# Optimization experiments

Measured on AMD Instinct MI355X. Metric: run time of the kernel, lower is better.

## Reference

```python
import jax, jax.numpy as jnp
import numpy as np

K = 3          # kernel size
STRIDE = 1
PAD = 1
DIL = 1
K2 = K * K


def setup_inputs() -> dict:
    key = jax.random.key(0)
    ks = jax.random.split(key, 5)
    B, Cin, Cout, H, W = 8, 128, 128, 64, 64
    x = jax.random.normal(ks[0], (B, Cin, H, W), jnp.float32)
    # conv_offset_mask: Conv2d(Cin, 3*dg*K*K=27, 3x3). Original inits to zero;
    # use small random weights so offsets are nonzero sub-pixel shifts.
    w_off = jax.random.normal(ks[1], (3 * K2, Cin, K, K), jnp.float32) * 0.05
    b_off = jax.random.normal(ks[2], (3 * K2,), jnp.float32) * 0.1
    weight = jax.random.normal(ks[3], (Cout, Cin, K, K), jnp.float32) / np.sqrt(Cin * K2)
    bias = jax.random.normal(ks[4], (Cout,), jnp.float32) * 0.1
    return dict(x=x, w_off=w_off, b_off=b_off, weight=weight, bias=bias)


def _conv(x, w, b):
    y = jax.lax.conv_general_dilated(
        x, w, (STRIDE, STRIDE), [(PAD, PAD), (PAD, PAD)],
        dimension_numbers=('NCHW', 'OIHW', 'NCHW'))
    return y + b[None, :, None, None]


def _sample_one(xb, pyb, pxb, mb):
    Cin, Hin, Win = xb.shape
    y0 = jnp.floor(pyb)
    x0 = jnp.floor(pxb)
    wy = pyb - y0   # fractional weights
    wx = pxb - x0
    y0i = y0.astype(jnp.int32)
    x0i = x0.astype(jnp.int32)
    xf = xb.reshape(Cin, -1)

    def g(yi, xi):
        valid = ((yi >= 0) & (yi < Hin) & (xi >= 0) & (xi < Win)).astype(xb.dtype)
        idx = jnp.clip(yi, 0, Hin - 1) * Win + jnp.clip(xi, 0, Win - 1)
        return xf[:, idx] * valid[None]   # [Cin,K2,Ho,Wo]

    v = (g(y0i, x0i) * ((1 - wy) * (1 - wx))[None]
         + g(y0i, x0i + 1) * ((1 - wy) * wx)[None]
         + g(y0i + 1, x0i) * (wy * (1 - wx))[None]
         + g(y0i + 1, x0i + 1) * (wy * wx)[None])
    return v * mb[None]   # modulated columns [Cin,K2,Ho,Wo]


def reference(x, w_off, b_off, weight, bias):
    B, Cin, Hin, Win = x.shape
    Cout = weight.shape[0]
    om = _conv(x, w_off, b_off)                 # [B, 3*K2, Ho, Wo]
    dy = om[:, :K2]
    dx = om[:, K2:2 * K2]
    m = jax.nn.sigmoid(om[:, 2 * K2:])          # modulation mask
    Ho, Wo = dy.shape[2], dy.shape[3]
    kh = jnp.repeat(jnp.arange(K), K)           # [K2] kernel row per tap
    kw = jnp.tile(jnp.arange(K), K)             # [K2] kernel col per tap
    grid_y = jnp.arange(Ho) * STRIDE - PAD
    grid_x = jnp.arange(Wo) * STRIDE - PAD
    py = dy + grid_y[None, None, :, None] + (kh * DIL)[None, :, None, None]
    px = dx + grid_x[None, None, None, :] + (kw * DIL)[None, :, None, None]
    cols = jax.vmap(_sample_one)(x, py, px, m)  # [B,Cin,K2,Ho,Wo]
    out = jnp.einsum('bckhw,ock->bohw', cols, weight.reshape(Cout, Cin, K2))
    return out + bias[None, :, None, None]
```

## Files before the change

kernel.cpp:

```cpp
#include <hip/hip_runtime.h>
#include <math.h>

#define BATCH 8
#define CIN   128
#define COUT  128
#define HH    64
#define WW    64
#define OC    27
#define KDIM  1152
#define CST   228

typedef unsigned short u16;
typedef unsigned int   u32;
typedef __attribute__((ext_vector_type(8))) short bf16x8;
typedef __attribute__((ext_vector_type(4))) float f32x4;

__device__ __forceinline__ float b2f(u16 u) {
    return __uint_as_float((u32)u << 16);
}
__device__ __forceinline__ u16 f2b(float f) {
    u32 u = __float_as_uint(f);
    return (u16)((u + 0x7fffu + ((u >> 16) & 1u)) >> 16);
}
__device__ __forceinline__ float blo(u32 u) { return __uint_as_float(u << 16); }
__device__ __forceinline__ float bhi(u32 u) { return __uint_as_float(u & 0xffff0000u); }
__device__ __forceinline__ u32 cvtpk(float lo, float hi) {
    u32 r;
    asm("v_cvt_pk_bf16_f32 %0, %1, %2" : "=v"(r) : "v"(lo), "v"(hi));
    return r;
}
__device__ __forceinline__ bf16x8 pack8(u32 a, u32 b, u32 c, u32 d) {
    union { u32 u[4]; bf16x8 v; } z;
    z.u[0] = a; z.u[1] = b; z.u[2] = c; z.u[3] = d;
    return z.v;
}

__device__ __forceinline__ int xswiz(int o, int K) { return (o & 7) * K + (o >> 3); }

__global__ __launch_bounds__(256) void k_prep(const float* __restrict__ x,
                                              const float* __restrict__ weight,
                                              const float* __restrict__ w_off,
                                              u16* __restrict__ xtb,
                                              u16* __restrict__ wbf,
                                              u16* __restrict__ wop) {
    __shared__ float tile[64][65];
    int gbid = blockIdx.x;
    int t = threadIdx.x;
    if (gbid < 1024) {
        int bid = xswiz(gbid, 128);
        int b   = bid >> 7;
        int c0  = ((bid >> 6) & 1) << 6;
        int hw0 = (bid & 63) << 6;
        int ln  = t & 63;
        int cq  = t >> 6;
#pragma unroll
        for (int r = 0; r < 16; ++r) {
            int c_l = cq * 16 + r;
            tile[c_l][ln] = x[(((size_t)(b * CIN + c0 + c_l)) << 12) + hw0 + ln];
        }
        __syncthreads();
#pragma unroll
        for (int r = 0; r < 16; ++r) {
            int hw_w = cq * 16 + r;
            xtb[((size_t)(b << 12) + hw0 + hw_w) * 128 + c0 + ln] = f2b(tile[ln][hw_w]);
        }
    } else if (gbid < 1600) {
        int tid = (gbid - 1024) * 256 + t;
        int j  = tid & 7;
        int l  = (tid >> 3) & 63;
        int ni = (tid >> 9) & 7;
        int s  = (tid >> 12) & 3;
        int t9 = tid >> 14;
        int co = ni * 16 + (l & 15);
        int ci = s * 32 + ((l >> 4) << 3) + j;
        wbf[tid] = f2b(weight[co * KDIM + ci * 9 + t9]);
    } else {
        int tid = (gbid - 1600) * 256 + t;
        int j   = tid & 7;
        int l   = (tid >> 3) & 63;
        int ni  = (tid >> 9) & 1;
        int sg  = (tid >> 10) & 3;
        int rest = tid >> 12;
        int t9  = rest % 9;
        int split = rest / 9;
        int co = ni * 16 + (l & 15);
        int ci = sg * 32 + ((l >> 4) << 3) + j;
        float val = (co < OC) ? w_off[co * KDIM + ci * 9 + t9] : 0.f;
        u16 hi = f2b(val);
        u16 lo = f2b(val - b2f(hi));
        wop[tid] = split ? lo : hi;
    }
}

__global__ __launch_bounds__(512, 4) void k_fused(const float* __restrict__ x,
                                                  const u16* __restrict__ xtb,
                                                  const u16* __restrict__ wop,
                                                  const u16* __restrict__ wbf,
                                                  const float* __restrict__ b_off,
                                                  const float* __restrict__ bias,
                                                  float* __restrict__ out) {
    __shared__ __align__(16) char smem[73904];
    float* Xf  = (float*)smem;
    float* red = (float*)(smem + 58368);
    float* omf = (float*)(smem + 66560);

    const int t  = threadIdx.x;
    const int lb = xswiz(blockIdx.x, 64);
    const int b  = lb >> 6;
    const int h  = lb & 63;
    const int l    = t & 63;
    const int wv   = t >> 6;
    const int l15  = l & 15;
    const int lg   = l >> 4;

    {
        const int ntile = wv & 3;
        const int kgrp  = wv >> 2;

        if (t < 192) {
            int ci = t & 63, row = t >> 6;
            int idx = ci * CST + row * 68 + (((ci >> 3) & 3) << 3) + 64;
            *(float4*)(Xf + idx) = make_float4(0.f, 0.f, 0.f, 0.f);
        }

        f32x4 acc0 = {0.f, 0.f, 0.f, 0.f};
        f32x4 acc1 = {0.f, 0.f, 0.f, 0.f};
        float4 st_[6];

        auto stageA_load = [&](int half) {
#pragma unroll
            for (int it = 0; it < 6; ++it) {
                int slot = t + it * 512;
                int pair = slot >> 4, ln16 = slot & 15;
                int row = pair >> 6, ci = pair & 63;
                int grow = h - 1 + row;
                float4 v = make_float4(0.f, 0.f, 0.f, 0.f);
                if ((unsigned)grow < 64u)
                    v = *(const float4*)(x + (((size_t)(b * CIN + half * 64 + ci)) << 12)
                                           + (grow << 6) + ln16 * 4);
                st_[it] = v;
            }
        };
        auto stageA_store = [&]() {
#pragma unroll
            for (int it = 0; it < 6; ++it) {
                int slot = t + it * 512;
                int pair = slot >> 4, ln16 = slot & 15;
                int row = pair >> 6, ci = pair & 63;
                int idx = ci * CST + row * 68 + (((ci >> 3) & 3) << 3) + ln16 * 4;
                *(float4*)(Xf + idx) = st_[it];
            }
        };
        auto kloopA = [&](int half) {
            for (int tap = 0; tap < 9; ++tap) {
                int kh = tap / 3, kw = tap - kh * 3;
                int gw = ntile * 16 + kw - 1 + l15;
                int px = (gw < 0) ? 64 : ((gw > 63) ? 65 : gw);
                int ci0 = kgrp * 32 + (lg << 3);
                int base = ci0 * CST + kh * 68 + (((ci0 >> 3) & 3) << 3) + px;
                float f0 = Xf[base], f1 = Xf[base + CST];
                float f2 = Xf[base + 2 * CST], f3 = Xf[base + 3 * CST];
                float f4 = Xf[base + 4 * CST], f5 = Xf[base + 5 * CST];
                float f6 = Xf[base + 6 * CST], f7 = Xf[base + 7 * CST];
                u32 h0 = cvtpk(f0, f1), h1 = cvtpk(f2, f3);
                u32 h2 = cvtpk(f4, f5), h3 = cvtpk(f6, f7);
                u32 l0 = cvtpk(f0 - blo(h0), f1 - bhi(h0));
                u32 l1 = cvtpk(f2 - blo(h1), f3 - bhi(h1));
                u32 l2 = cvtpk(f4 - blo(h2), f5 - bhi(h2));
                u32 l3 = cvtpk(f6 - blo(h3), f7 - bhi(h3));
                bf16x8 ah = pack8(h0, h1, h2, h3);
                bf16x8 al = pack8(l0, l1, l2, l3);
                int sg = half * 2 + kgrp;
                const u16* B = wop + (((tap * 4 + sg) * 2) << 9) + (l << 3);
                bf16x8 wh0 = *(const bf16x8*)(B);
                bf16x8 wh1 = *(const bf16x8*)(B + 512);
                bf16x8 wl0 = *(const bf16x8*)(B + 36864);
                bf16x8 wl1 = *(const bf16x8*)(B + 36864 + 512);
                __builtin_amdgcn_s_setprio(1);
                acc0 = __builtin_amdgcn_mfma_f32_16x16x32_bf16(wh0, ah, acc0, 0, 0, 0);
                acc1 = __builtin_amdgcn_mfma_f32_16x16x32_bf16(wh1, ah, acc1, 0, 0, 0);
                acc0 = __builtin_amdgcn_mfma_f32_16x16x32_bf16(wl0, ah, acc0, 0, 0, 0);
                acc1 = __builtin_amdgcn_mfma_f32_16x16x32_bf16(wl1, ah, acc1, 0, 0, 0);
                acc0 = __builtin_amdgcn_mfma_f32_16x16x32_bf16(wh0, al, acc0, 0, 0, 0);
                acc1 = __builtin_amdgcn_mfma_f32_16x16x32_bf16(wh1, al, acc1, 0, 0, 0);
                __builtin_amdgcn_s_setprio(0);
            }
        };

        stageA_load(0);
        stageA_store();
        __syncthreads();
        stageA_load(1);
        kloopA(0);
        __syncthreads();
        stageA_store();
        __syncthreads();
        kloopA(1);

        if (kgrp) {
            float* rp = red + (((ntile << 6) + l) << 3);
            *(f32x4*)rp = acc0;
            *(f32x4*)(rp + 4) = acc1;
        }
        __syncthreads();
        if (!kgrp) {
            const float* rp = red + (((ntile << 6) + l) << 3);
            acc0 += *(const f32x4*)rp;
            acc1 += *(const f32x4*)(rp + 4);
            int px = ntile * 16 + l15;
            int co0 = lg << 2;
#pragma unroll
            for (int r = 0; r < 4; ++r)
                omf[(co0 + r) * 68 + px] = acc0[r] + b_off[co0 + r];
            int co1 = 16 + (lg << 2);
#pragma unroll
            for (int r = 0; r < 4; ++r) {
                int co = co1 + r;
                if (co < OC) {
                    float v = acc1[r] + b_off[co];
                    if (co >= 18) v = 1.f / (1.f + expf(-v));
                    omf[co * 68 + px] = v;
                }
            }
        }
        __syncthreads();
    }

    float (*w4)[4] = (float (*)[4])(smem + 32768);
    u32* idxp = (u32*)(smem + 41984);

    for (int i = t; i < 576; i += 512) {
        int p  = i / 9;
        int tt = i - p * 9;
        float dy = omf[tt * 68 + p];
        float dx = omf[(9 + tt) * 68 + p];
        float m  = omf[(18 + tt) * 68 + p];
        float py = dy + (float)(h - 1 + tt / 3);
        float px = dx + (float)(p - 1 + tt % 3);
        float y0f = floorf(py), x0f = floorf(px);
        float wy = py - y0f, wx = px - x0f;
        int y0 = (int)y0f, x0 = (int)x0f;
        int y1 = y0 + 1,   x1 = x0 + 1;
        float vy0 = ((unsigned)y0 < 64u) ? 1.f : 0.f;
        float vy1 = ((unsigned)y1 < 64u) ? 1.f : 0.f;
        float vx0 = ((unsigned)x0 < 64u) ? 1.f : 0.f;
        float vx1 = ((unsigned)x1 < 64u) ? 1.f : 0.f;
        w4[i][0] = (1.f - wy) * (1.f - wx) * m * vy0 * vx0;
        w4[i][1] = (1.f - wy) * wx         * m * vy0 * vx1;
        w4[i][2] = wy         * (1.f - wx) * m * vy1 * vx0;
        w4[i][3] = wy         * wx         * m * vy1 * vx1;
        int y0c = min(max(y0, 0), 63);
        int y1c = min(max(y1, 0), 63);
        int x0c = min(max(x0, 0), 63);
        int x1c = min(max(x1, 0), 63);
        idxp[i] = (u32)y0c | ((u32)y1c << 8) | ((u32)x0c << 16) | ((u32)x1c << 24);
    }
    __syncthreads();

    f32x4 acc[4][2];
#pragma unroll
    for (int pt = 0; pt < 4; ++pt)
#pragma unroll
        for (int nt = 0; nt < 2; ++nt) acc[pt][nt] = (f32x4){0.f, 0.f, 0.f, 0.f};

    const int grp  = t >> 8;
    const int tl   = t & 255;
    const int l2   = tl & 63;
    const int wv2  = tl >> 6;
    const int row0 = l2 & 15;
    const int kg   = l2 >> 4;

    const int sp = tl >> 2;
    const int sc = tl & 3;
    const u16* xb = xtb + ((size_t)b << 19);

    uint4 g_[2][4];

    auto sample_load = [&](int tt) {
        u32 pk = idxp[sp * 9 + tt];
        int y0 = pk & 255, y1 = (pk >> 8) & 255;
        int x0 = (pk >> 16) & 255, x1 = pk >> 24;
        int d1 = (x1 - x0) << 7;
        const u16* p0 = xb + (((y0 << 6) | x0) << 7) + grp * 64 + sc * 8;
        const u16* p1 = xb + (((y1 << 6) | x0) << 7) + grp * 64 + sc * 8;
        g_[0][0] = *(const uint4*)(p0);
        g_[0][1] = *(const uint4*)(p0 + d1);
        g_[0][2] = *(const uint4*)(p1);
        g_[0][3] = *(const uint4*)(p1 + d1);
        g_[1][0] = *(const uint4*)(p0 + 32);
        g_[1][1] = *(const uint4*)(p0 + d1 + 32);
        g_[1][2] = *(const uint4*)(p1 + 32);
        g_[1][3] = *(const uint4*)(p1 + d1 + 32);
    };

    auto sample_finish = [&](int tt, int buf) {
        int pi = sp * 9 + tt;
        float4 W = *(const float4*)(&w4[pi][0]);
        u16* dst = (u16*)(smem + buf * 16384);
#pragma unroll
        for (int k = 0; k < 2; ++k) {
            uint4 a00 = g_[k][0], a01 = g_[k][1], a10 = g_[k][2], a11 = g_[k][3];
            uint4 ow;
            {
                float e0 = W.x * blo(a00.x) + W.y * blo(a01.x) + W.z * blo(a10.x) + W.w * blo(a11.x);
                float e1 = W.x * bhi(a00.x) + W.y * bhi(a01.x) + W.z * bhi(a10.x) + W.w * bhi(a11.x);
                ow.x = cvtpk(e0, e1);
            }
            {
                float e0 = W.x * blo(a00.y) + W.y * blo(a01.y) + W.z * blo(a10.y) + W.w * blo(a11.y);
                float e1 = W.x * bhi(a00.y) + W.y * bhi(a01.y) + W.z * bhi(a10.y) + W.w * bhi(a11.y);
                ow.y = cvtpk(e0, e1);
            }
            {
                float e0 = W.x * blo(a00.z) + W.y * blo(a01.z) + W.z * blo(a10.z) + W.w * blo(a11.z);
                float e1 = W.x * bhi(a00.z) + W.y * bhi(a01.z) + W.z * bhi(a10.z) + W.w * bhi(a11.z);
                ow.z = cvtpk(e0, e1);
            }
            {
                float e0 = W.x * blo(a00.w) + W.y * blo(a01.w) + W.z * blo(a10.w) + W.w * blo(a11.w);
                float e1 = W.x * bhi(a00.w) + W.y * bhi(a01.w) + W.z * bhi(a10.w) + W.w * bhi(a11.w);
                ow.w = cvtpk(e0, e1);
            }
            int q16 = (grp * 8 + k * 4 + sc) ^ (sp & 15);
            *(uint4*)((char*)dst + (sp << 8) + (q16 << 4)) = ow;
        }
    };

    auto domfma = [&](int t9, int buf) {
        const char* Ab = (const char*)(smem + buf * 16384);
#pragma unroll
        for (int shalf = 0; shalf < 2; ++shalf) {
            int s = grp * 2 + shalf;
            int q = s * 4 + kg;
            int sw = (q ^ row0) << 4;
            bf16x8 a[4];
#pragma unroll
            for (int pt = 0; pt < 4; ++pt)
                a[pt] = *(const bf16x8*)(Ab + ((pt * 16 + row0) << 8) + sw);
            const u16* B = wbf + ((size_t)t9 << 14) + (s << 12) + (wv2 << 10) + (l2 << 3);
            bf16x8 b0 = *(const bf16x8*)(B);
            bf16x8 b1 = *(const bf16x8*)(B + 512);
            __builtin_amdgcn_s_setprio(1);
#pragma unroll
            for (int pt = 0; pt < 4; ++pt) {
                acc[pt][0] = __builtin_amdgcn_mfma_f32_16x16x32_bf16(a[pt], b0, acc[pt][0], 0, 0, 0);
                acc[pt][1] = __builtin_amdgcn_mfma_f32_16x16x32_bf16(a[pt], b1, acc[pt][1], 0, 0, 0);
            }
            __builtin_amdgcn_s_setprio(0);
        }
    };

    sample_load(0);
    sample_finish(0, 0);
    __syncthreads();
    for (int tt = 0; tt < 9; ++tt) {
        if (tt < 8) sample_load(tt + 1);
        domfma(tt, tt & 1);
        if (tt < 8) sample_finish(tt + 1, (tt + 1) & 1);
        __syncthreads();
    }

    float* outs = (float*)smem;
    if (grp) {
#pragma unroll
        for (int pt = 0; pt < 4; ++pt)
#pragma unroll
            for (int nt = 0; nt < 2; ++nt) {
                int co  = wv2 * 32 + nt * 16 + row0;
                int pxq = pt * 4 + kg;
                *(f32x4*)((char*)outs + (co << 8) + ((pxq ^ (co & 7)) << 4)) = acc[pt][nt];
            }
    }
    __syncthreads();
    if (!grp) {
#pragma unroll
        for (int pt = 0; pt < 4; ++pt)
#pragma unroll
            for (int nt = 0; nt < 2; ++nt) {
                int co  = wv2 * 32 + nt * 16 + row0;
                int pxq = pt * 4 + kg;
                char* ad = (char*)outs + (co << 8) + ((pxq ^ (co & 7)) << 4);
                f32x4 v = *(const f32x4*)ad;
                *(f32x4*)ad = v + acc[pt][nt];
            }
    }
    __syncthreads();
    {
        int co = t >> 2, qt = t & 3;
        float bb = bias[co];
        float* og = out + (((size_t)(b * COUT + co)) << 12) + (h << 6);
#pragma unroll
        for (int j = 0; j < 4; ++j) {
            int pxq = qt * 4 + j;
            f32x4 v = *(const f32x4*)((const char*)outs + (co << 8) + ((pxq ^ (co & 7)) << 4));
            float4 r = make_float4(v.x + bb, v.y + bb, v.z + bb, v.w + bb);
            *reinterpret_cast<float4*>(og + pxq * 4) = r;
        }
    }
}

extern "C" void kernel_launch(void* const* d_in, const int* in_sizes, int n_in,
                              void* d_out, int out_size, void* d_ws, size_t ws_size,
                              hipStream_t stream) {
    const float* x      = (const float*)d_in[0];
    const float* w_off  = (const float*)d_in[1];
    const float* b_off  = (const float*)d_in[2];
    const float* weight = (const float*)d_in[3];
    const float* bias   = (const float*)d_in[4];
    float* out = (float*)d_out;

    u16* xtb = (u16*)d_ws;
    u16* wbf = xtb + 4194304;
    u16* wop = wbf + 147456;

    k_prep<<<1888, 256, 0, stream>>>(x, weight, w_off, xtb, wbf, wop);
    k_fused<<<512, 512, 0, stream>>>(x, xtb, wop, wbf, b_off, bias, out);
}
```

Before: 48.43 us.

## Split each output row across two 256-thread blocks to double grid size

Each block now handles half of an output row (32 pixels) with 256 threads instead of a full row with 512 threads, giving 1024 blocks and about half the shared memory per block. The offset-conv stage loads a halo-padded 40-wide strip. The main MFMA stage drops the cross-group K split, so each wave covers the full channel depth and writes results straight from registers, with no shared-memory reduction. The aim is more blocks in flight and better latency hiding. In exchange, halo columns are loaded twice and each wave does a longer serial K loop.

```diff
diff --git a/kernel.cpp b/kernel.cpp
--- a/kernel.cpp
+++ b/kernel.cpp
@@ -8,7 +8,7 @@
 #define WW    64
 #define OC    27
 #define KDIM  1152
-#define CST   228
+#define CST   132
 
 typedef unsigned short u16;
 typedef unsigned int   u32;
@@ -92,72 +92,73 @@
     }
 }
 
-__global__ __launch_bounds__(512, 4) void k_fused(const float* __restrict__ x,
+__global__ __launch_bounds__(256, 4) void k_fused(const float* __restrict__ x,
                                                   const u16* __restrict__ xtb,
                                                   const u16* __restrict__ wop,
                                                   const u16* __restrict__ wbf,
                                                   const float* __restrict__ b_off,
                                                   const float* __restrict__ bias,
                                                   float* __restrict__ out) {
-    __shared__ __align__(16) char smem[73904];
+    __shared__ __align__(16) char smem[37888];
     float* Xf  = (float*)smem;
-    float* red = (float*)(smem + 58368);
-    float* omf = (float*)(smem + 66560);
-
-    const int t  = threadIdx.x;
-    const int lb = xswiz(blockIdx.x, 64);
-    const int b  = lb >> 6;
-    const int h  = lb & 63;
+    float* red = (float*)(smem + 33792);
+    float* omf = (float*)(smem + 22144);
+
+    const int t    = threadIdx.x;
+    const int lb   = xswiz(blockIdx.x, 128);
+    const int b    = lb >> 7;
+    const int h    = (lb >> 1) & 63;
+    const int half = lb & 1;
+    const int w0   = half << 5;
     const int l    = t & 63;
     const int wv   = t >> 6;
     const int l15  = l & 15;
     const int lg   = l >> 4;
 
     {
-        const int ntile = wv & 3;
-        const int kgrp  = wv >> 2;
-
-        if (t < 192) {
-            int ci = t & 63, row = t >> 6;
-            int idx = ci * CST + row * 68 + (((ci >> 3) & 3) << 3) + 64;
-            *(float4*)(Xf + idx) = make_float4(0.f, 0.f, 0.f, 0.f);
-        }
+        const int ntile = wv & 1;
+        const int kgrp  = wv >> 1;
 
         f32x4 acc0 = {0.f, 0.f, 0.f, 0.f};
         f32x4 acc1 = {0.f, 0.f, 0.f, 0.f};
-        float4 st_[6];
-
-        auto stageA_load = [&](int half) {
-#pragma unroll
-            for (int it = 0; it < 6; ++it) {
-                int slot = t + it * 512;
-                int pair = slot >> 4, ln16 = slot & 15;
-                int row = pair >> 6, ci = pair & 63;
-                int grow = h - 1 + row;
-                float4 v = make_float4(0.f, 0.f, 0.f, 0.f);
-                if ((unsigned)grow < 64u)
-                    v = *(const float4*)(x + (((size_t)(b * CIN + half * 64 + ci)) << 12)
-                                           + (grow << 6) + ln16 * 4);
-                st_[it] = v;
+        float4 st_[8];
+
+        auto stageA_load = [&](int rnd) {
+#pragma unroll
+            for (int it = 0; it < 8; ++it) {
+                int i = t + it * 256;
+                st_[it] = make_float4(0.f, 0.f, 0.f, 0.f);
+                if (i < 1920) {
+                    int k  = i % 10;
+                    int pr = i / 10;
+                    int ci = pr & 63, row = pr >> 6;
+                    int grow = h - 1 + row;
+                    int g0   = w0 - 4 + k * 4;
+                    if ((unsigned)grow < 64u && (unsigned)g0 <= 60u)
+                        st_[it] = *(const float4*)(x + (((size_t)(b * CIN + rnd * 64 + ci)) << 12)
+                                                     + (grow << 6) + g0);
+                }
             }
         };
         auto stageA_store = [&]() {
 #pragma unroll
-            for (int it = 0; it < 6; ++it) {
-                int slot = t + it * 512;
-                int pair = slot >> 4, ln16 = slot & 15;
-                int row = pair >> 6, ci = pair & 63;
-                int idx = ci * CST + row * 68 + (((ci >> 3) & 3) << 3) + ln16 * 4;
-                *(float4*)(Xf + idx) = st_[it];
+            for (int it = 0; it < 8; ++it) {
+                int i = t + it * 256;
+                if (i < 1920) {
+                    int k  = i % 10;
+                    int pr = i / 10;
+                    int ci = pr & 63, row = pr >> 6;
+                    int idx = ci * CST + row * 40 + (((ci >> 3) & 3) << 2) + k * 4;
+                    *(float4*)(Xf + idx) = st_[it];
+                }
             }
         };
-        auto kloopA = [&](int half) {
+        auto kloopA = [&](int rnd) {
             for (int tap = 0; tap < 9; ++tap) {
                 int kh = tap / 3, kw = tap - kh * 3;
-                int gw = ntile * 16 + kw - 1 + l15;
-                int px = (gw < 0) ? 64 : ((gw > 63) ? 65 : gw);
-                int ci0 = kgrp * 32 + (lg << 3);
-                int base = ci0 * CST + kh * 68 + (((ci0 >> 3) & 3) << 3) + px;
+                int slot = ntile * 16 + l15 + kw + 3;
+                int ci0  = kgrp * 32 + (lg << 3);
+                int base = ci0 * CST + kh * 40 + (lg << 2) + slot;
                 float f0 = Xf[base], f1 = Xf[base + CST];
                 float f2 = Xf[base + 2 * CST], f3 = Xf[base + 3 * CST];
                 float f4 = Xf[base + 4 * CST], f5 = Xf[base + 5 * CST];
@@ -170,7 +171,7 @@
                 u32 l3 = cvtpk(f6 - blo(h3), f7 - bhi(h3));
                 bf16x8 ah = pack8(h0, h1, h2, h3);
                 bf16x8 al = pack8(l0, l1, l2, l3);
-                int sg = half * 2 + kgrp;
+                int sg = rnd * 2 + kgrp;
                 const u16* B = wop + (((tap * 4 + sg) * 2) << 9) + (l << 3);
                 bf16x8 wh0 = *(const bf16x8*)(B);
                 bf16x8 wh1 = *(const bf16x8*)(B + 512);
@@ -196,6 +197,7 @@
         stageA_store();
         __syncthreads();
         kloopA(1);
+        __syncthreads();
 
         if (kgrp) {
             float* rp = red + (((ntile << 6) + l) << 3);
@@ -211,7 +213,7 @@
             int co0 = lg << 2;
 #pragma unroll
             for (int r = 0; r < 4; ++r)
-                omf[(co0 + r) * 68 + px] = acc0[r] + b_off[co0 + r];
+                omf[(co0 + r) * 36 + px] = acc0[r] + b_off[co0 + r];
             int co1 = 16 + (lg << 2);
 #pragma unroll
             for (int r = 0; r < 4; ++r) {
@@ -219,24 +221,24 @@
                 if (co < OC) {
                     float v = acc1[r] + b_off[co];
                     if (co >= 18) v = 1.f / (1.f + expf(-v));
-                    omf[co * 68 + px] = v;
+                    omf[co * 36 + px] = v;
                 }
             }
         }
         __syncthreads();
     }
 
-    float (*w4)[4] = (float (*)[4])(smem + 32768);
-    u32* idxp = (u32*)(smem + 41984);
-
-    for (int i = t; i < 576; i += 512) {
+    float (*w4)[4] = (float (*)[4])(smem + 16384);
+    u32* idxp = (u32*)(smem + 20992);
+
+    for (int i = t; i < 288; i += 256) {
         int p  = i / 9;
         int tt = i - p * 9;
-        float dy = omf[tt * 68 + p];
-        float dx = omf[(9 + tt) * 68 + p];
-        float m  = omf[(18 + tt) * 68 + p];
+        float dy = omf[tt * 36 + p];
+        float dx = omf[(9 + tt) * 36 + p];
+        float m  = omf[(18 + tt) * 36 + p];
         float py = dy + (float)(h - 1 + tt / 3);
-        float px = dx + (float)(p - 1 + tt % 3);
+        float px = dx + (float)(w0 + p - 1 + tt % 3);
         float y0f = floorf(py), x0f = floorf(px);
         float wy = py - y0f, wx = px - x0f;
         int y0 = (int)y0f, x0 = (int)x0f;
@@ -257,21 +259,18 @@
     }
     __syncthreads();
 
-    f32x4 acc[4][2];
-#pragma unroll
-    for (int pt = 0; pt < 4; ++pt)
+    f32x4 acc[2][2];
+#pragma unroll
+    for (int pt = 0; pt < 2; ++pt)
 #pragma unroll
         for (int nt = 0; nt < 2; ++nt) acc[pt][nt] = (f32x4){0.f, 0.f, 0.f, 0.f};
 
-    const int grp  = t >> 8;
-    const int tl   = t & 255;
-    const int l2   = tl & 63;
-    const int wv2  = tl >> 6;
-    const int row0 = l2 & 15;
-    const int kg   = l2 >> 4;
-
-    const int sp = tl >> 2;
-    const int sc = tl & 3;
+    const int wv2  = wv;
+    const int row0 = l15;
+    const int kg   = lg;
+
+    const int sp = t >> 3;
+    const int sc = t & 7;
     const u16* xb = xtb + ((size_t)b << 19);
 
     uint4 g_[2][4];
@@ -281,22 +280,22 @@
         int y0 = pk & 255, y1 = (pk >> 8) & 255;
         int x0 = (pk >> 16) & 255, x1 = pk >> 24;
         int d1 = (x1 - x0) << 7;
-        const u16* p0 = xb + (((y0 << 6) | x0) << 7) + grp * 64 + sc * 8;
-        const u16* p1 = xb + (((y1 << 6) | x0) << 7) + grp * 64 + sc * 8;
+        const u16* p0 = xb + ((((y0 << 6) | x0) << 7)) + sc * 8;
+        const u16* p1 = xb + ((((y1 << 6) | x0) << 7)) + sc * 8;
         g_[0][0] = *(const uint4*)(p0);
         g_[0][1] = *(const uint4*)(p0 + d1);
         g_[0][2] = *(const uint4*)(p1);
         g_[0][3] = *(const uint4*)(p1 + d1);
-        g_[1][0] = *(const uint4*)(p0 + 32);
-        g_[1][1] = *(const uint4*)(p0 + d1 + 32);
-        g_[1][2] = *(const uint4*)(p1 + 32);
-        g_[1][3] = *(const uint4*)(p1 + d1 + 32);
+        g_[1][0] = *(const uint4*)(p0 + 64);
+        g_[1][1] = *(const uint4*)(p0 + d1 + 64);
+        g_[1][2] = *(const uint4*)(p1 + 64);
+        g_[1][3] = *(const uint4*)(p1 + d1 + 64);
     };
 
     auto sample_finish = [&](int tt, int buf) {
         int pi = sp * 9 + tt;
         float4 W = *(const float4*)(&w4[pi][0]);
-        u16* dst = (u16*)(smem + buf * 16384);
+        u16* dst = (u16*)(smem + buf * 8192);
 #pragma unroll
         for (int k = 0; k < 2; ++k) {
             uint4 a00 = g_[k][0], a01 = g_[k][1], a10 = g_[k][2], a11 = g_[k][3];
@@ -321,31 +320,27 @@
                 float e1 = W.x * bhi(a00.w) + W.y * bhi(a01.w) + W.z * bhi(a10.w) + W.w * bhi(a11.w);
                 ow.w = cvtpk(e0, e1);
             }
-            int q16 = (grp * 8 + k * 4 + sc) ^ (sp & 15);
+            int q16 = (k * 8 + sc) ^ (sp & 15);
             *(uint4*)((char*)dst + (sp << 8) + (q16 << 4)) = ow;
         }
     };
 
     auto domfma = [&](int t9, int buf) {
-        const char* Ab = (const char*)(smem + buf * 16384);
-#pragma unroll
-        for (int shalf = 0; shalf < 2; ++shalf) {
-            int s = grp * 2 + shalf;
+        const char* Ab = (const char*)(smem + buf * 8192);
+#pragma unroll
+        for (int s = 0; s < 4; ++s) {
             int q = s * 4 + kg;
             int sw = (q ^ row0) << 4;
-            bf16x8 a[4];
-#pragma unroll
-            for (int pt = 0; pt < 4; ++pt)
-                a[pt] = *(const bf16x8*)(Ab + ((pt * 16 + row0) << 8) + sw);
-            const u16* B = wbf + ((size_t)t9 << 14) + (s << 12) + (wv2 << 10) + (l2 << 3);
+            bf16x8 a0 = *(const bf16x8*)(Ab + (row0 << 8) + sw);
+            bf16x8 a1 = *(const bf16x8*)(Ab + ((16 + row0) << 8) + sw);
+            const u16* B = wbf + ((size_t)t9 << 14) + (s << 12) + (wv2 << 10) + (l << 3);
             bf16x8 b0 = *(const bf16x8*)(B);
             bf16x8 b1 = *(const bf16x8*)(B + 512);
             __builtin_amdgcn_s_setprio(1);
-#pragma unroll
-            for (int pt = 0; pt < 4; ++pt) {
-                acc[pt][0] = __builtin_amdgcn_mfma_f32_16x16x32_bf16(a[pt], b0, acc[pt][0], 0, 0, 0);
-                acc[pt][1] = __builtin_amdgcn_mfma_f32_16x16x32_bf16(a[pt], b1, acc[pt][1], 0, 0, 0);
-            }
+            acc[0][0] = __builtin_amdgcn_mfma_f32_16x16x32_bf16(a0, b0, acc[0][0], 0, 0, 0);
+            acc[0][1] = __builtin_amdgcn_mfma_f32_16x16x32_bf16(a0, b1, acc[0][1], 0, 0, 0);
+            acc[1][0] = __builtin_amdgcn_mfma_f32_16x16x32_bf16(a1, b0, acc[1][0], 0, 0, 0);
+            acc[1][1] = __builtin_amdgcn_mfma_f32_16x16x32_bf16(a1, b1, acc[1][1], 0, 0, 0);
             __builtin_amdgcn_s_setprio(0);
         }
     };
@@ -360,39 +355,15 @@
         __syncthreads();
     }
 
-    float* outs = (float*)smem;
-    if (grp) {
-#pragma unroll
-        for (int pt = 0; pt < 4; ++pt)
-#pragma unroll
-            for (int nt = 0; nt < 2; ++nt) {
-                int co  = wv2 * 32 + nt * 16 + row0;
-                int pxq = pt * 4 + kg;
-                *(f32x4*)((char*)outs + (co << 8) + ((pxq ^ (co & 7)) << 4)) = acc[pt][nt];
-            }
-    }
-    __syncthreads();
-    if (!grp) {
-#pragma unroll
-        for (int pt = 0; pt < 4; ++pt)
-#pragma unroll
-            for (int nt = 0; nt < 2; ++nt) {
-                int co  = wv2 * 32 + nt * 16 + row0;
-                int pxq = pt * 4 + kg;
-                char* ad = (char*)outs + (co << 8) + ((pxq ^ (co & 7)) << 4);
-                f32x4 v = *(const f32x4*)ad;
-                *(f32x4*)ad = v + acc[pt][nt];
-            }
-    }
-    __syncthreads();
-    {
-        int co = t >> 2, qt = t & 3;
+#pragma unroll
+    for (int nt = 0; nt < 2; ++nt) {
+        int co = wv2 * 32 + nt * 16 + row0;
         float bb = bias[co];
-        float* og = out + (((size_t)(b * COUT + co)) << 12) + (h << 6);
-#pragma unroll
-        for (int j = 0; j < 4; ++j) {
-            int pxq = qt * 4 + j;
-            f32x4 v = *(const f32x4*)((const char*)outs + (co << 8) + ((pxq ^ (co & 7)) << 4));
+        float* og = out + (((size_t)(b * COUT + co)) << 12) + (h << 6) + w0;
+#pragma unroll
+        for (int pt = 0; pt < 2; ++pt) {
+            int pxq = pt * 4 + kg;
+            f32x4 v = acc[pt][nt];
             float4 r = make_float4(v.x + bb, v.y + bb, v.z + bb, v.w + bb);
             *reinterpret_cast<float4*>(og + pxq * 4) = r;
         }
@@ -414,5 +385,5 @@
     u16* wop = wbf + 147456;
 
     k_prep<<<1888, 256, 0, stream>>>(x, weight, w_off, xtb, wbf, wop);
-    k_fused<<<512, 512, 0, stream>>>(x, xtb, wop, wbf, b_off, bias, out);
-}
+    k_fused<<<1024, 256, 0, stream>>>(x, xtb, wop, wbf, b_off, bias, out);
+}
```

Result: slower. 50.45 us (+4.2%).

## Deepen gather prefetch to two stages and preload B fragments into registers

Applied to the files above, without the earlier changes.

The sampling loop now keeps two register sets of gathered input loads, so tap t+2 is fetched while tap t+1 is blended and tap t is fed to MFMA. Weight B fragments for the next tap are loaded into registers ahead of the MFMA loop instead of inside it. The loop is unrolled by two with fixed buffer indices. Launch bounds drop from 4 to 2 blocks per CU to make room for the extra registers, which trades occupancy for deeper latency hiding.

```diff
diff --git a/kernel.cpp b/kernel.cpp
--- a/kernel.cpp
+++ b/kernel.cpp
@@ -92,7 +92,7 @@
     }
 }
 
-__global__ __launch_bounds__(512, 4) void k_fused(const float* __restrict__ x,
+__global__ __launch_bounds__(512, 2) void k_fused(const float* __restrict__ x,
                                                   const u16* __restrict__ xtb,
                                                   const u16* __restrict__ wop,
                                                   const u16* __restrict__ wbf,
@@ -274,32 +274,41 @@
     const int sc = tl & 3;
     const u16* xb = xtb + ((size_t)b << 19);
 
-    uint4 g_[2][4];
-
-    auto sample_load = [&](int tt) {
+    uint4 g0[2][4], g1[2][4];
+    bf16x8 Bc[4];
+
+    auto bloadB = [&](int t9) {
+        const u16* Bp = wbf + ((size_t)t9 << 14) + (wv2 << 10) + (l2 << 3);
+        Bc[0] = *(const bf16x8*)(Bp + ((grp * 2 + 0) << 12));
+        Bc[1] = *(const bf16x8*)(Bp + ((grp * 2 + 0) << 12) + 512);
+        Bc[2] = *(const bf16x8*)(Bp + ((grp * 2 + 1) << 12));
+        Bc[3] = *(const bf16x8*)(Bp + ((grp * 2 + 1) << 12) + 512);
+    };
+
+    auto sample_load = [&](int tt, uint4 (&g)[2][4]) {
         u32 pk = idxp[sp * 9 + tt];
         int y0 = pk & 255, y1 = (pk >> 8) & 255;
         int x0 = (pk >> 16) & 255, x1 = pk >> 24;
         int d1 = (x1 - x0) << 7;
         const u16* p0 = xb + (((y0 << 6) | x0) << 7) + grp * 64 + sc * 8;
         const u16* p1 = xb + (((y1 << 6) | x0) << 7) + grp * 64 + sc * 8;
-        g_[0][0] = *(const uint4*)(p0);
-        g_[0][1] = *(const uint4*)(p0 + d1);
-        g_[0][2] = *(const uint4*)(p1);
-        g_[0][3] = *(const uint4*)(p1 + d1);
-        g_[1][0] = *(const uint4*)(p0 + 32);
-        g_[1][1] = *(const uint4*)(p0 + d1 + 32);
-        g_[1][2] = *(const uint4*)(p1 + 32);
-        g_[1][3] = *(const uint4*)(p1 + d1 + 32);
+        g[0][0] = *(const uint4*)(p0);
+        g[0][1] = *(const uint4*)(p0 + d1);
+        g[0][2] = *(const uint4*)(p1);
+        g[0][3] = *(const uint4*)(p1 + d1);
+        g[1][0] = *(const uint4*)(p0 + 32);
+        g[1][1] = *(const uint4*)(p0 + d1 + 32);
+        g[1][2] = *(const uint4*)(p1 + 32);
+        g[1][3] = *(const uint4*)(p1 + d1 + 32);
     };
 
-    auto sample_finish = [&](int tt, int buf) {
+    auto sample_finish = [&](int tt, const uint4 (&g)[2][4], int buf) {
         int pi = sp * 9 + tt;
         float4 W = *(const float4*)(&w4[pi][0]);
         u16* dst = (u16*)(smem + buf * 16384);
 #pragma unroll
         for (int k = 0; k < 2; ++k) {
-            uint4 a00 = g_[k][0], a01 = g_[k][1], a10 = g_[k][2], a11 = g_[k][3];
+            uint4 a00 = g[k][0], a01 = g[k][1], a10 = g[k][2], a11 = g[k][3];
             uint4 ow;
             {
                 float e0 = W.x * blo(a00.x) + W.y * blo(a01.x) + W.z * blo(a10.x) + W.w * blo(a11.x);
@@ -326,7 +335,7 @@
         }
     };
 
-    auto domfma = [&](int t9, int buf) {
+    auto domfma = [&](int buf) {
         const char* Ab = (const char*)(smem + buf * 16384);
 #pragma unroll
         for (int shalf = 0; shalf < 2; ++shalf) {
@@ -337,9 +346,8 @@
 #pragma unroll
             for (int pt = 0; pt < 4; ++pt)
                 a[pt] = *(const bf16x8*)(Ab + ((pt * 16 + row0) << 8) + sw);
-            const u16* B = wbf + ((size_t)t9 << 14) + (s << 12) + (wv2 << 10) + (l2 << 3);
-            bf16x8 b0 = *(const bf16x8*)(B);
-            bf16x8 b1 = *(const bf16x8*)(B + 512);
+            bf16x8 b0 = Bc[shalf * 2];
+            bf16x8 b1 = Bc[shalf * 2 + 1];
             __builtin_amdgcn_s_setprio(1);
 #pragma unroll
             for (int pt = 0; pt < 4; ++pt) {
@@ -350,15 +358,25 @@
         }
     };
 
-    sample_load(0);
-    sample_finish(0, 0);
+    bloadB(0);
+    sample_load(0, g0);
+    sample_load(1, g1);
+    sample_finish(0, g0, 0);
     __syncthreads();
-    for (int tt = 0; tt < 9; ++tt) {
-        if (tt < 8) sample_load(tt + 1);
-        domfma(tt, tt & 1);
-        if (tt < 8) sample_finish(tt + 1, (tt + 1) & 1);
-        __syncthreads();
-    }
+    for (int base = 0; base < 8; base += 2) {
+        domfma(0);
+        bloadB(base + 1);
+        sample_load(base + 2, g0);
+        sample_finish(base + 1, g1, 1);
+        __syncthreads();
+        domfma(1);
+        bloadB(base + 2);
+        if (base < 6) sample_load(base + 3, g1);
+        sample_finish(base + 2, g0, 0);
+        __syncthreads();
+    }
+    domfma(0);
+    __syncthreads();
 
     float* outs = (float*)smem;
     if (grp) {
```

After: 61.31 us. 26.6% more time.
